# Kernel optimization log

Hardware: AMD Instinct MI355X
Metric: run time of the kernel (lower is better)

## Reference

```python
import jax, jax.numpy as jnp
import numpy as np

NUM_HEADS = 8

def setup_inputs() -> dict:
    key = jax.random.key(0)
    ks = jax.random.split(key, 6)
    B, S, D, K = 2, 2048, 512, 64
    x = jax.random.normal(ks[0], (B, S, D), dtype=jnp.float32)
    routes = jax.random.randint(ks[1], (S, K), 0, S, dtype=jnp.int32)
    distances = jax.random.uniform(ks[2], (S, S), dtype=jnp.float32)
    W_in = jax.random.normal(ks[3], (D, D), dtype=jnp.float32) * (1.0 / np.sqrt(D))
    W_out = jax.random.normal(ks[4], (D, D), dtype=jnp.float32) * (1.0 / np.sqrt(D))
    b_out = jnp.zeros((D,), dtype=jnp.float32)
    return {"x": x, "routes": routes, "distances": distances,
            "W_in": W_in, "W_out": W_out, "b_out": b_out}

def reference(x, routes, distances, W_in, W_out, b_out):
    # x: [B,S,D]; routes: [S,K] int gather table; distances: [S,S]
    B, S, D = x.shape
    H = NUM_HEADS
    hd = D // H
    K = routes.shape[1]
    # in_proj (torch Linear, no bias): y = x @ W^T
    h = jnp.einsum('bsd,ed->bse', x, W_in).reshape(B, S, H, hd)
    # gather fusion windows via precomputed routes: [B,S,K,H,hd]
    gathered = h[:, routes]
    # weighted fusion: weights from precomputed Cantor distance matrix
    d = jnp.take_along_axis(distances, routes.astype(jnp.int32), axis=1)  # [S,K]
    w = jax.nn.softmax(-d, axis=-1)  # normalized fusion weights
    fused = jnp.einsum('sk,bskhd->bshd', w, gathered)  # [B,S,H,hd]
    fused = fused.reshape(B, S, D)
    # out_proj + residual (dropout is identity in eval)
    out = jnp.einsum('bsd,ed->bse', fused, W_out) + b_out
    return out + x
```

## Files before the change

### kernel.cpp

```cpp
#include <hip/hip_runtime.h>
#include <hip/hip_bf16.h>

#define S_DIM 2048
#define D_DIM 512
#define B_DIM 2
#define K_RT  64

typedef __attribute__((ext_vector_type(8))) short short8;
typedef __attribute__((ext_vector_type(4))) float f32x4;

static __device__ __forceinline__ float bf16lo_to_f(unsigned u) {
    union { unsigned u; float f; } c; c.u = u << 16; return c.f;
}
static __device__ __forceinline__ float bf16hi_to_f(unsigned u) {
    union { unsigned u; float f; } c; c.u = u & 0xffff0000u; return c.f;
}
static __device__ __forceinline__ unsigned short f_to_bf16(float f) {
    union { float f; unsigned u; } c; c.f = f;
    unsigned u = c.u;
    u += 0x7fffu + ((u >> 16) & 1u);
    return (unsigned short)(u >> 16);
}

__global__ __launch_bounds__(256) void cast_all(
    const float* __restrict__ x, const float* __restrict__ Wi, const float* __restrict__ Wo,
    unsigned short* __restrict__ xb, unsigned short* __restrict__ wib, unsigned short* __restrict__ wob)
{
    const int g = blockIdx.x * 256 + threadIdx.x;
    const int NX = B_DIM * S_DIM * D_DIM / 4;
    const int NW = D_DIM * D_DIM / 4;
    const float* src; unsigned short* dst; int off;
    if (g < NX)           { src = x;  dst = xb;  off = g; }
    else if (g < NX + NW) { src = Wi; dst = wib; off = g - NX; }
    else                  { src = Wo; dst = wob; off = g - NX - NW; }
    const float4 v = ((const float4*)src)[off];
    ushort4 o;
    o.x = f_to_bf16(v.x); o.y = f_to_bf16(v.y);
    o.z = f_to_bf16(v.z); o.w = f_to_bf16(v.w);
    ((ushort4*)dst)[off] = o;
}

#define GBM 64
#define GBN 64
#define GBK 32
#define LROW 40

__global__ __launch_bounds__(256) void gemm_bt_bf16(
    const unsigned short* __restrict__ A,
    const unsigned short* __restrict__ B,
    unsigned short* __restrict__ Cb,
    float* __restrict__ Cf,
    const float* __restrict__ bias, const float* __restrict__ residual,
    int M, int N, int K)
{
    __shared__ unsigned short As[GBM * LROW];
    __shared__ unsigned short Bs[GBN * LROW];

    const int tid  = threadIdx.x;
    const int lane = tid & 63;
    const int wv   = tid >> 6;
    const int wm   = (wv & 1) * 32;
    const int wn   = (wv >> 1) * 32;
    const int m0   = blockIdx.y * GBM;
    const int n0   = blockIdx.x * GBN;

    const int lr = tid >> 2;
    const int lc = (tid & 3) * 8;

    const int mi = lane & 15;
    const int kg = lane >> 4;

    f32x4 acc[2][2] = {};

    for (int k0 = 0; k0 < K; k0 += GBK) {
        const uint4 a4 = *(const uint4*)(A + (size_t)(m0 + lr) * K + k0 + lc);
        const uint4 b4 = *(const uint4*)(B + (size_t)(n0 + lr) * K + k0 + lc);
        *(uint4*)(As + lr * LROW + lc) = a4;
        *(uint4*)(Bs + lr * LROW + lc) = b4;
        __syncthreads();

        short8 af0 = *(const short8*)(As + (wm +      mi) * LROW + kg * 8);
        short8 af1 = *(const short8*)(As + (wm + 16 + mi) * LROW + kg * 8);
        short8 bf0 = *(const short8*)(Bs + (wn +      mi) * LROW + kg * 8);
        short8 bf1 = *(const short8*)(Bs + (wn + 16 + mi) * LROW + kg * 8);

        acc[0][0] = __builtin_amdgcn_mfma_f32_16x16x32_bf16(af0, bf0, acc[0][0], 0, 0, 0);
        acc[0][1] = __builtin_amdgcn_mfma_f32_16x16x32_bf16(af0, bf1, acc[0][1], 0, 0, 0);
        acc[1][0] = __builtin_amdgcn_mfma_f32_16x16x32_bf16(af1, bf0, acc[1][0], 0, 0, 0);
        acc[1][1] = __builtin_amdgcn_mfma_f32_16x16x32_bf16(af1, bf1, acc[1][1], 0, 0, 0);
        __syncthreads();
    }

    const int rb  = (lane >> 4) * 4;
    const int col = lane & 15;
    #pragma unroll
    for (int i = 0; i < 2; ++i) {
        #pragma unroll
        for (int j = 0; j < 2; ++j) {
            #pragma unroll
            for (int r = 0; r < 4; ++r) {
                const int m = m0 + wm + i * 16 + rb + r;
                const int n = n0 + wn + j * 16 + col;
                const float v = acc[i][j][r];
                if (Cf) {
                    Cf[(size_t)m * N + n] = v + bias[n] + residual[(size_t)m * N + n];
                } else {
                    Cb[(size_t)m * N + n] = f_to_bf16(v);
                }
            }
        }
    }
}

__global__ __launch_bounds__(256) void fuse_gather(
    const unsigned short* __restrict__ h, const int* __restrict__ routes,
    const float* __restrict__ distances, unsigned short* __restrict__ fused)
{
    const int tid  = threadIdx.x;
    const int lane = tid & 63;
    const int wv   = tid >> 6;
    const int s    = blockIdx.x * 4 + wv;
    const int b    = blockIdx.y;

    const int rt = routes[s * K_RT + lane];
    const float v = -distances[(size_t)s * S_DIM + rt];
    float mx = v;
    #pragma unroll
    for (int off = 32; off >= 1; off >>= 1) mx = fmaxf(mx, __shfl_xor(mx, off, 64));
    const float e = __expf(v - mx);
    float sum = e;
    #pragma unroll
    for (int off = 32; off >= 1; off >>= 1) sum += __shfl_xor(sum, off, 64);
    const float wl = e / sum;

    const unsigned short* hb = h + (size_t)b * S_DIM * D_DIM;
    float acc[8] = {};
    #pragma unroll 4
    for (int k = 0; k < 64; ++k) {
        const int   rk = __shfl(rt, k, 64);
        const float wk = __shfl(wl, k, 64);
        const uint4 p = *(const uint4*)(hb + (size_t)rk * D_DIM + lane * 8);
        acc[0] = fmaf(wk, bf16lo_to_f(p.x), acc[0]);
        acc[1] = fmaf(wk, bf16hi_to_f(p.x), acc[1]);
        acc[2] = fmaf(wk, bf16lo_to_f(p.y), acc[2]);
        acc[3] = fmaf(wk, bf16hi_to_f(p.y), acc[3]);
        acc[4] = fmaf(wk, bf16lo_to_f(p.z), acc[4]);
        acc[5] = fmaf(wk, bf16hi_to_f(p.z), acc[5]);
        acc[6] = fmaf(wk, bf16lo_to_f(p.w), acc[6]);
        acc[7] = fmaf(wk, bf16hi_to_f(p.w), acc[7]);
    }
    uint4 o;
    o.x = (unsigned)f_to_bf16(acc[0]) | ((unsigned)f_to_bf16(acc[1]) << 16);
    o.y = (unsigned)f_to_bf16(acc[2]) | ((unsigned)f_to_bf16(acc[3]) << 16);
    o.z = (unsigned)f_to_bf16(acc[4]) | ((unsigned)f_to_bf16(acc[5]) << 16);
    o.w = (unsigned)f_to_bf16(acc[6]) | ((unsigned)f_to_bf16(acc[7]) << 16);
    *(uint4*)(fused + ((size_t)b * S_DIM + s) * D_DIM + lane * 8) = o;
}

extern "C" void kernel_launch(void* const* d_in, const int* in_sizes, int n_in,
                              void* d_out, int out_size, void* d_ws, size_t ws_size,
                              hipStream_t stream) {
    const float* x         = (const float*)d_in[0];
    const int*   routes    = (const int*)  d_in[1];
    const float* distances = (const float*)d_in[2];
    const float* W_in      = (const float*)d_in[3];
    const float* W_out     = (const float*)d_in[4];
    const float* b_out     = (const float*)d_in[5];
    float* out = (float*)d_out;

    const int M = B_DIM * S_DIM;

    unsigned short* xb  = (unsigned short*)d_ws;
    unsigned short* wib = xb  + (size_t)M * D_DIM;
    unsigned short* wob = wib + (size_t)D_DIM * D_DIM;
    unsigned short* hb  = wob + (size_t)D_DIM * D_DIM;
    unsigned short* fb  = hb  + (size_t)M * D_DIM;

    cast_all<<<2560, 256, 0, stream>>>(x, W_in, W_out, xb, wib, wob);
    gemm_bt_bf16<<<dim3(D_DIM / GBN, M / GBM), 256, 0, stream>>>(
        xb, wib, hb, nullptr, nullptr, nullptr, M, D_DIM, D_DIM);
    fuse_gather<<<dim3(S_DIM / 4, B_DIM), 256, 0, stream>>>(hb, routes, distances, fb);
    gemm_bt_bf16<<<dim3(D_DIM / GBN, M / GBM), 256, 0, stream>>>(
        fb, wob, nullptr, out, b_out, x, M, D_DIM, D_DIM);
}
```

Before: 121.9 us.

## Precompute softmax weights in prep kernel and load GEMM tiles directly to LDS

The softmax over route distances moves out of fuse_gather into the cast kernel, which now also writes per-row weights, so each batch no longer recomputes them. The GEMM stages A/B tiles with global_load_lds (direct global-to-LDS DMA) instead of going through registers, which drops the padded LDS row stride. It is templated on the output type, and the gather loop unroll goes from 4 to 8. The unpadded 32-element LDS rows may raise bank conflicts on the fragment reads.

```diff
diff --git a/kernel.cpp b/kernel.cpp
--- a/kernel.cpp
+++ b/kernel.cpp
@@ -5,9 +5,13 @@
 #define D_DIM 512
 #define B_DIM 2
 #define K_RT  64
+#define M_DIM 4096
 
 typedef __attribute__((ext_vector_type(8))) short short8;
 typedef __attribute__((ext_vector_type(4))) float f32x4;
+typedef unsigned int u32;
+#define AS1 __attribute__((address_space(1)))
+#define AS3 __attribute__((address_space(3)))
 
 static __device__ __forceinline__ float bf16lo_to_f(unsigned u) {
     union { unsigned u; float f; } c; c.u = u << 16; return c.f;
@@ -21,40 +25,62 @@
     u += 0x7fffu + ((u >> 16) & 1u);
     return (unsigned short)(u >> 16);
 }
-
-__global__ __launch_bounds__(256) void cast_all(
-    const float* __restrict__ x, const float* __restrict__ Wi, const float* __restrict__ Wo,
-    unsigned short* __restrict__ xb, unsigned short* __restrict__ wib, unsigned short* __restrict__ wob)
+static __device__ __forceinline__ unsigned pk2(float a, float b) {
+    return (unsigned)f_to_bf16(a) | ((unsigned)f_to_bf16(b) << 16);
+}
+
+__global__ __launch_bounds__(256) void prep(
+    const float* __restrict__ x, const int* __restrict__ routes,
+    const float* __restrict__ distances,
+    const float* __restrict__ Wi, const float* __restrict__ Wo,
+    unsigned short* __restrict__ xb, unsigned short* __restrict__ wib,
+    unsigned short* __restrict__ wob, float* __restrict__ w)
 {
-    const int g = blockIdx.x * 256 + threadIdx.x;
-    const int NX = B_DIM * S_DIM * D_DIM / 4;
-    const int NW = D_DIM * D_DIM / 4;
-    const float* src; unsigned short* dst; int off;
-    if (g < NX)           { src = x;  dst = xb;  off = g; }
-    else if (g < NX + NW) { src = Wi; dst = wib; off = g - NX; }
-    else                  { src = Wo; dst = wob; off = g - NX - NW; }
-    const float4 v = ((const float4*)src)[off];
-    ushort4 o;
-    o.x = f_to_bf16(v.x); o.y = f_to_bf16(v.y);
-    o.z = f_to_bf16(v.z); o.w = f_to_bf16(v.w);
-    ((ushort4*)dst)[off] = o;
+    const int blk = blockIdx.x;
+    if (blk < 512) {
+        const int lane = threadIdx.x & 63;
+        const int wv   = threadIdx.x >> 6;
+        const int s    = blk * 4 + wv;
+        const int rt   = routes[s * K_RT + lane];
+        const float v  = -distances[(size_t)s * S_DIM + rt];
+        float mx = v;
+        #pragma unroll
+        for (int off = 32; off >= 1; off >>= 1) mx = fmaxf(mx, __shfl_xor(mx, off, 64));
+        const float e = __expf(v - mx);
+        float sum = e;
+        #pragma unroll
+        for (int off = 32; off >= 1; off >>= 1) sum += __shfl_xor(sum, off, 64);
+        w[s * K_RT + lane] = e / sum;
+    } else {
+        const int g = (blk - 512) * 256 + threadIdx.x;
+        const int NX = M_DIM * D_DIM / 4;
+        const int NW = D_DIM * D_DIM / 4;
+        const float* src; unsigned short* dst; int off;
+        if (g < NX)           { src = x;  dst = xb;  off = g; }
+        else if (g < NX + NW) { src = Wi; dst = wib; off = g - NX; }
+        else                  { src = Wo; dst = wob; off = g - NX - NW; }
+        const float4 v = ((const float4*)src)[off];
+        ushort4 o;
+        o.x = f_to_bf16(v.x); o.y = f_to_bf16(v.y);
+        o.z = f_to_bf16(v.z); o.w = f_to_bf16(v.w);
+        ((ushort4*)dst)[off] = o;
+    }
 }
 
 #define GBM 64
 #define GBN 64
 #define GBK 32
-#define LROW 40
-
-__global__ __launch_bounds__(256) void gemm_bt_bf16(
+
+template<bool OUTF32>
+__global__ __launch_bounds__(256) void gemm_bt(
     const unsigned short* __restrict__ A,
     const unsigned short* __restrict__ B,
-    unsigned short* __restrict__ Cb,
-    float* __restrict__ Cf,
+    void* __restrict__ Cv,
     const float* __restrict__ bias, const float* __restrict__ residual,
     int M, int N, int K)
 {
-    __shared__ unsigned short As[GBM * LROW];
-    __shared__ unsigned short Bs[GBN * LROW];
+    __shared__ unsigned short As[GBM * GBK];
+    __shared__ unsigned short Bs[GBN * GBK];
 
     const int tid  = threadIdx.x;
     const int lane = tid & 63;
@@ -64,8 +90,8 @@
     const int m0   = blockIdx.y * GBM;
     const int n0   = blockIdx.x * GBN;
 
-    const int lr = tid >> 2;
-    const int lc = (tid & 3) * 8;
+    const int srow  = wv * 16 + (lane >> 2);
+    const int skoff = (lane & 3) * 8;
 
     const int mi = lane & 15;
     const int kg = lane >> 4;
@@ -73,16 +99,18 @@
     f32x4 acc[2][2] = {};
 
     for (int k0 = 0; k0 < K; k0 += GBK) {
-        const uint4 a4 = *(const uint4*)(A + (size_t)(m0 + lr) * K + k0 + lc);
-        const uint4 b4 = *(const uint4*)(B + (size_t)(n0 + lr) * K + k0 + lc);
-        *(uint4*)(As + lr * LROW + lc) = a4;
-        *(uint4*)(Bs + lr * LROW + lc) = b4;
+        __builtin_amdgcn_global_load_lds(
+            (const AS1 u32*)(A + (size_t)(m0 + srow) * K + k0 + skoff),
+            (AS3 u32*)(As + wv * 16 * GBK), 16, 0, 0);
+        __builtin_amdgcn_global_load_lds(
+            (const AS1 u32*)(B + (size_t)(n0 + srow) * K + k0 + skoff),
+            (AS3 u32*)(Bs + wv * 16 * GBK), 16, 0, 0);
         __syncthreads();
 
-        short8 af0 = *(const short8*)(As + (wm +      mi) * LROW + kg * 8);
-        short8 af1 = *(const short8*)(As + (wm + 16 + mi) * LROW + kg * 8);
-        short8 bf0 = *(const short8*)(Bs + (wn +      mi) * LROW + kg * 8);
-        short8 bf1 = *(const short8*)(Bs + (wn + 16 + mi) * LROW + kg * 8);
+        short8 af0 = *(const short8*)(As + (wm +      mi) * GBK + kg * 8);
+        short8 af1 = *(const short8*)(As + (wm + 16 + mi) * GBK + kg * 8);
+        short8 bf0 = *(const short8*)(Bs + (wn +      mi) * GBK + kg * 8);
+        short8 bf1 = *(const short8*)(Bs + (wn + 16 + mi) * GBK + kg * 8);
 
         acc[0][0] = __builtin_amdgcn_mfma_f32_16x16x32_bf16(af0, bf0, acc[0][0], 0, 0, 0);
         acc[0][1] = __builtin_amdgcn_mfma_f32_16x16x32_bf16(af0, bf1, acc[0][1], 0, 0, 0);
@@ -102,10 +130,10 @@
                 const int m = m0 + wm + i * 16 + rb + r;
                 const int n = n0 + wn + j * 16 + col;
                 const float v = acc[i][j][r];
-                if (Cf) {
-                    Cf[(size_t)m * N + n] = v + bias[n] + residual[(size_t)m * N + n];
+                if (OUTF32) {
+                    ((float*)Cv)[(size_t)m * N + n] = v + bias[n] + residual[(size_t)m * N + n];
                 } else {
-                    Cb[(size_t)m * N + n] = f_to_bf16(v);
+                    ((unsigned short*)Cv)[(size_t)m * N + n] = f_to_bf16(v);
                 }
             }
         }
@@ -114,7 +142,7 @@
 
 __global__ __launch_bounds__(256) void fuse_gather(
     const unsigned short* __restrict__ h, const int* __restrict__ routes,
-    const float* __restrict__ distances, unsigned short* __restrict__ fused)
+    const float* __restrict__ w, unsigned short* __restrict__ fused)
 {
     const int tid  = threadIdx.x;
     const int lane = tid & 63;
@@ -122,20 +150,12 @@
     const int s    = blockIdx.x * 4 + wv;
     const int b    = blockIdx.y;
 
-    const int rt = routes[s * K_RT + lane];
-    const float v = -distances[(size_t)s * S_DIM + rt];
-    float mx = v;
-    #pragma unroll
-    for (int off = 32; off >= 1; off >>= 1) mx = fmaxf(mx, __shfl_xor(mx, off, 64));
-    const float e = __expf(v - mx);
-    float sum = e;
-    #pragma unroll
-    for (int off = 32; off >= 1; off >>= 1) sum += __shfl_xor(sum, off, 64);
-    const float wl = e / sum;
+    const int   rt = routes[s * K_RT + lane];
+    const float wl = w[s * K_RT + lane];
 
     const unsigned short* hb = h + (size_t)b * S_DIM * D_DIM;
     float acc[8] = {};
-    #pragma unroll 4
+    #pragma unroll 8
     for (int k = 0; k < 64; ++k) {
         const int   rk = __shfl(rt, k, 64);
         const float wk = __shfl(wl, k, 64);
@@ -150,10 +170,10 @@
         acc[7] = fmaf(wk, bf16hi_to_f(p.w), acc[7]);
     }
     uint4 o;
-    o.x = (unsigned)f_to_bf16(acc[0]) | ((unsigned)f_to_bf16(acc[1]) << 16);
-    o.y = (unsigned)f_to_bf16(acc[2]) | ((unsigned)f_to_bf16(acc[3]) << 16);
-    o.z = (unsigned)f_to_bf16(acc[4]) | ((unsigned)f_to_bf16(acc[5]) << 16);
-    o.w = (unsigned)f_to_bf16(acc[6]) | ((unsigned)f_to_bf16(acc[7]) << 16);
+    o.x = pk2(acc[0], acc[1]);
+    o.y = pk2(acc[2], acc[3]);
+    o.z = pk2(acc[4], acc[5]);
+    o.w = pk2(acc[6], acc[7]);
     *(uint4*)(fused + ((size_t)b * S_DIM + s) * D_DIM + lane * 8) = o;
 }
 
@@ -168,18 +188,17 @@
     const float* b_out     = (const float*)d_in[5];
     float* out = (float*)d_out;
 
-    const int M = B_DIM * S_DIM;
-
     unsigned short* xb  = (unsigned short*)d_ws;
-    unsigned short* wib = xb  + (size_t)M * D_DIM;
+    unsigned short* wib = xb  + (size_t)M_DIM * D_DIM;
     unsigned short* wob = wib + (size_t)D_DIM * D_DIM;
     unsigned short* hb  = wob + (size_t)D_DIM * D_DIM;
-    unsigned short* fb  = hb  + (size_t)M * D_DIM;
-
-    cast_all<<<2560, 256, 0, stream>>>(x, W_in, W_out, xb, wib, wob);
-    gemm_bt_bf16<<<dim3(D_DIM / GBN, M / GBM), 256, 0, stream>>>(
-        xb, wib, hb, nullptr, nullptr, nullptr, M, D_DIM, D_DIM);
-    fuse_gather<<<dim3(S_DIM / 4, B_DIM), 256, 0, stream>>>(hb, routes, distances, fb);
-    gemm_bt_bf16<<<dim3(D_DIM / GBN, M / GBM), 256, 0, stream>>>(
-        fb, wob, nullptr, out, b_out, x, M, D_DIM, D_DIM);
-}
+    unsigned short* fb  = hb  + (size_t)M_DIM * D_DIM;
+    float*          w   = (float*)(fb + (size_t)M_DIM * D_DIM);
+
+    const dim3 ggrid(D_DIM / GBN, M_DIM / GBM);
+
+    prep<<<3072, 256, 0, stream>>>(x, routes, distances, W_in, W_out, xb, wib, wob, w);
+    gemm_bt<false><<<ggrid, 256, 0, stream>>>(xb, wib, hb, nullptr, nullptr, M_DIM, D_DIM, D_DIM);
+    fuse_gather<<<dim3(S_DIM / 4, B_DIM), 256, 0, stream>>>(hb, routes, w, fb);
+    gemm_bt<true><<<ggrid, 256, 0, stream>>>(fb, wob, out, b_out, x, M_DIM, D_DIM, D_DIM);
+}
```

New measurement: 121.1 us. Within noise of the previous version (-0.6%).
